# Performance work log

Hardware: AMD Instinct MI355X
Metric: run time of the kernel (lower is better)

The kernel has to match this reference:

```python
import jax, jax.numpy as jnp
import numpy as np

N_USERS, N_ITEMS, N_GROUPS = 20000, 20000, 2000
MAX_M, D, K, B = 20, 64, 2, 8192


def setup_inputs() -> dict:
    key = jax.random.key(0)
    ks = jax.random.split(key, 12)
    membership = jax.random.randint(ks[0], (N_GROUPS, MAX_M), 0, N_USERS)
    member_mask = jnp.zeros((N_GROUPS, MAX_M), jnp.float32)  # exp -> all-ones weights
    # binary group-member incidence consistent with membership (dedupes duplicates)
    hyper_graph = jnp.zeros((N_GROUPS, N_USERS), jnp.float32)
    hyper_graph = hyper_graph.at[jnp.arange(N_GROUPS)[:, None], membership].set(1.0)
    user_emb = 0.1 * jax.random.normal(ks[1], (N_USERS, D), jnp.float32)
    item_emb = 0.1 * jax.random.normal(ks[2], (N_ITEMS, D), jnp.float32)
    Wk = 0.05 * jax.random.normal(ks[3], (K, D, 2 * D), jnp.float32)
    bk = jnp.zeros((K, D), jnp.float32)
    p1w = 0.1 * jax.random.normal(ks[4], (16, D), jnp.float32)
    p1b = jnp.zeros((16,), jnp.float32)
    p2w = 0.1 * jax.random.normal(ks[5], (1, 16), jnp.float32)
    p2b = jnp.zeros((1,), jnp.float32)
    groups = jax.random.randint(ks[6], (B,), 0, N_GROUPS)
    items = jax.random.randint(ks[7], (B,), 0, N_ITEMS)
    return dict(groups=groups, items=items, membership=membership,
                member_mask=member_mask, hyper_graph=hyper_graph,
                user_emb=user_emb, item_emb=item_emb, Wk=Wk, bk=bk,
                p1w=p1w, p1b=p1b, p2w=p2w, p2b=p2b)


def _l2norm(x, eps=1e-12):
    return x / jnp.maximum(jnp.linalg.norm(x, axis=-1, keepdims=True), eps)


def reference(groups, items, membership, member_mask, hyper_graph,
              user_emb, item_emb, Wk, bk, p1w, p1b, p2w, p2b):
    # masked-mean group embedding from member users: [G, D]
    w = jnp.exp(member_mask)                                  # [G, M]
    g_users = user_emb[membership]                            # [G, M, D]
    emb = (g_users * w[..., None]).sum(1) / w.sum(1, keepdims=True)
    # group adjacency = common-member counts, zero diagonal
    adj = hyper_graph @ hyper_graph.T                         # [G, G]
    adj = adj - jnp.diag(jnp.diag(adj))
    # Vectorized set-intersection message: for binary H, common count == adj[i,j],
    # so sum_j adj[i,j] * mean(U[common(i,j)]) = sum_j (H_i * H_j) @ U (j != i)
    #                                          = (H * H.sum(0) - H) @ U
    deg = hyper_graph.sum(0)                                  # [n_users]
    neigh_member = (hyper_graph * deg[None, :] - hyper_graph) @ user_emb  # [G, D]
    for i in range(K):
        neigh_group = adj @ emb                               # [G, D]
        msg = neigh_group + neigh_member
        emb = jnp.concatenate([emb, msg], axis=1) @ Wk[i].T + bk[i]
        emb = _l2norm(emb)
    ge = emb[groups]                                          # [B, D]
    ie = item_emb[items]                                      # [B, D]
    h = jax.nn.relu((ge * ie) @ p1w.T + p1b)                  # [B, 16]
    return jax.nn.sigmoid(h @ p2w.T + p2b)                    # [B, 1]
```

## Files before the change

### kernel.cpp

```cpp
#include <hip/hip_runtime.h>
#include <math.h>

#define D 64
#define MAXM 20
#define CAP 32
#define CAPS 64
#define WPB 8
#define TPB 512

#define XOR_COMBINE4(v)                                        \
  do {                                                         \
    v.x += __shfl_xor(v.x, 16); v.x += __shfl_xor(v.x, 32);    \
    v.y += __shfl_xor(v.y, 16); v.y += __shfl_xor(v.y, 32);    \
    v.z += __shfl_xor(v.z, 16); v.z += __shfl_xor(v.z, 32);    \
    v.w += __shfl_xor(v.w, 16); v.w += __shfl_xor(v.w, 32);    \
  } while (0)

__global__ __launch_bounds__(TPB) void init_kernel(
    const int* __restrict__ membership, const float* __restrict__ member_mask,
    const float* __restrict__ user_emb, const int* __restrict__ groups,
    float* __restrict__ emb0, unsigned int* __restrict__ ufm,
    int* __restrict__ deg, int* __restrict__ inv,
    int* __restrict__ scnt, int* __restrict__ sidx, int G, int B) {
  const int w    = threadIdx.x >> 6;
  const int lane = threadIdx.x & 63;
  const int g    = blockIdx.x * WPB + w;
  const int sub  = lane >> 4, q = lane & 15;
  __shared__ int   mem_s[WPB][MAXM];
  __shared__ float wgt_s[WPB][MAXM];
  int*   mem = mem_s[w];
  float* wgt = wgt_s[w];
  if (g < G) {
    if (lane < MAXM) {
      mem[lane] = membership[g * MAXM + lane];
      wgt[lane] = expf(member_mask[g * MAXM + lane]);
    }
    float wsum = 0.f;
#pragma unroll
    for (int m = 0; m < MAXM; ++m) wsum += wgt[m];
    float4 acc = make_float4(0.f, 0.f, 0.f, 0.f);
#pragma unroll
    for (int it = 0; it < MAXM / 4; ++it) {
      const int m = it * 4 + sub;
      const float c = wgt[m];
      const float4 v = *(const float4*)(user_emb + (long)mem[m] * D + q * 4);
      acc.x += c * v.x; acc.y += c * v.y; acc.z += c * v.z; acc.w += c * v.w;
    }
    XOR_COMBINE4(acc);
    if (lane < 16) {
      const float iw = 1.f / wsum;
      float4 r = make_float4(acc.x * iw, acc.y * iw, acc.z * iw, acc.w * iw);
      ((float4*)(emb0 + (long)g * D))[q] = r;
    }
    bool uniq = false;
    if (lane < MAXM) {
      const int u = mem[lane];
      uniq = true;
      for (int m = 0; m < lane; ++m)
        if (mem[m] == u) uniq = false;
    }
    const unsigned long long bal = __ballot(uniq);
    if (lane == 0) ufm[g] = (unsigned int)bal;
    if (uniq) {
      const int u = mem[lane];
      const int pos = atomicAdd(&deg[u], 1);
      if (pos < CAP) inv[(long)u * CAP + pos] = g;
    }
  }
  const int nthreads = gridDim.x * TPB;
  for (int s = blockIdx.x * TPB + threadIdx.x; s < B; s += nthreads) {
    const int gg = groups[s];
    const int pos = atomicAdd(&scnt[gg], 1);
    if (pos < CAPS) sidx[gg * CAPS + pos] = s;
  }
}

__device__ __forceinline__ float update_core(
    const int* __restrict__ membership, const unsigned int* __restrict__ ufm,
    const int* __restrict__ deg, const int* __restrict__ inv,
    const float* __restrict__ user_emb, float* __restrict__ nm, int compute_nm,
    const float* __restrict__ Wk, const float* __restrict__ bk, int k,
    const float* __restrict__ cur, int g, int lane,
    int* mem, float* coef, float* e_sh, float* ms_sh, int* nbr) {
  const int sub = lane >> 4, q = lane & 15;
  if (lane < MAXM) mem[lane] = membership[g * MAXM + lane];
  const unsigned int um = ufm[g];
  const float ein = cur[(long)g * D + lane];
  e_sh[lane] = ein;

  int d = 0, u = 0;
  const bool uq = (lane < MAXM) && ((um >> lane) & 1u);
  if (uq) { u = mem[lane]; d = deg[u]; }
  if (lane < MAXM) coef[lane] = uq ? (float)(d - 1) : 0.f;
  const int dc = d < CAP ? d : CAP;
  int incl = dc;
#pragma unroll
  for (int off = 1; off < 64; off <<= 1) {
    const int v = __shfl_up(incl, off);
    if (lane >= off) incl += v;
  }
  const int total = __shfl(incl, 63);
  const int base = incl - dc;
  for (int i = 0; i < dc; ++i) nbr[base + i] = inv[(long)u * CAP + i];
  const int padc = (8 - (total & 7)) & 7;
  if (lane < padc) nbr[total + lane] = g;

  const int T8 = total + padc;
  float4 a0 = make_float4(0.f, 0.f, 0.f, 0.f);
  float4 a1 = make_float4(0.f, 0.f, 0.f, 0.f);
  for (int i = 0; i < T8; i += 8) {
    const int r0 = nbr[i + sub];
    const int r1 = nbr[i + 4 + sub];
    const float4 v0 = *(const float4*)(cur + (long)r0 * D + q * 4);
    const float4 v1 = *(const float4*)(cur + (long)r1 * D + q * 4);
    a0.x += v0.x; a0.y += v0.y; a0.z += v0.z; a0.w += v0.w;
    a1.x += v1.x; a1.y += v1.y; a1.z += v1.z; a1.w += v1.w;
  }
  float4 ng4 = make_float4(a0.x + a1.x, a0.y + a1.y, a0.z + a1.z, a0.w + a1.w);
  XOR_COMBINE4(ng4);

  float4 nm4 = make_float4(0.f, 0.f, 0.f, 0.f);
  if (compute_nm) {
#pragma unroll
    for (int it = 0; it < MAXM / 4; ++it) {
      const int m = it * 4 + sub;
      const float c = coef[m];
      const float4 v = *(const float4*)(user_emb + (long)mem[m] * D + q * 4);
      nm4.x += c * v.x; nm4.y += c * v.y; nm4.z += c * v.z; nm4.w += c * v.w;
    }
    XOR_COMBINE4(nm4);
    if (lane < 16) ((float4*)(nm + (long)g * D))[q] = nm4;
  }
  if (lane < 16) {
    const float4 nmv4 =
        compute_nm ? nm4 : ((const float4*)(nm + (long)g * D))[q];
    const float alpha = (float)__popc(um) + (float)padc;
    const float4 e4 = ((const float4*)e_sh)[q];
    float4 ms4;
    ms4.x = ng4.x + nmv4.x - alpha * e4.x;
    ms4.y = ng4.y + nmv4.y - alpha * e4.y;
    ms4.z = ng4.z + nmv4.z - alpha * e4.z;
    ms4.w = ng4.w + nmv4.w - alpha * e4.w;
    ((float4*)ms_sh)[q] = ms4;
  }

  const float4* W4 = (const float4*)(Wk + ((long)k * D + lane) * (2 * D));
  const float4* e4p = (const float4*)e_sh;
  const float4* m4p = (const float4*)ms_sh;
  float o = bk[k * D + lane];
#pragma unroll
  for (int j = 0; j < 16; ++j) {
    const float4 a = e4p[j], wv = W4[j];
    o += a.x * wv.x + a.y * wv.y + a.z * wv.z + a.w * wv.w;
  }
#pragma unroll
  for (int j = 0; j < 16; ++j) {
    const float4 a = m4p[j], wv = W4[16 + j];
    o += a.x * wv.x + a.y * wv.y + a.z * wv.z + a.w * wv.w;
  }
  float ss = o * o;
#pragma unroll
  for (int sh = 32; sh; sh >>= 1) ss += __shfl_xor(ss, sh);
  return o * (1.f / fmaxf(sqrtf(ss), 1e-12f));
}

__global__ __launch_bounds__(TPB) void upd_kernel(
    const int* __restrict__ membership, const unsigned int* __restrict__ ufm,
    const int* __restrict__ deg, const int* __restrict__ inv,
    const float* __restrict__ user_emb, float* __restrict__ nm, int compute_nm,
    const float* __restrict__ Wk, const float* __restrict__ bk, int k,
    const float* __restrict__ cur, float* __restrict__ nxt, int G) {
  const int w = threadIdx.x >> 6, lane = threadIdx.x & 63;
  const int g0 = blockIdx.x * WPB + w;
  const int g = g0 < G ? g0 : G - 1;
  __shared__ int   mem_s[WPB][MAXM];
  __shared__ float coef_s[WPB][MAXM];
  __shared__ float e_s[WPB][D], ms_s[WPB][D];
  __shared__ int   nbr_s[WPB][MAXM * CAP + 8];
  const float o = update_core(membership, ufm, deg, inv, user_emb, nm,
                              compute_nm, Wk, bk, k, cur, g, lane,
                              mem_s[w], coef_s[w], e_s[w], ms_s[w], nbr_s[w]);
  if (g0 < G) nxt[(long)g0 * D + lane] = o;
}

__global__ __launch_bounds__(TPB) void upd_head_kernel(
    const int* __restrict__ membership, const unsigned int* __restrict__ ufm,
    const int* __restrict__ deg, const int* __restrict__ inv,
    const float* __restrict__ user_emb, float* __restrict__ nm, int compute_nm,
    const float* __restrict__ Wk, const float* __restrict__ bk, int k,
    const float* __restrict__ cur,
    const int* __restrict__ scnt, const int* __restrict__ sidx,
    const int* __restrict__ items, const float* __restrict__ item_emb,
    const float* __restrict__ p1w, const float* __restrict__ p1b,
    const float* __restrict__ p2w, const float* __restrict__ p2b,
    float* __restrict__ out, int G) {
  const int w = threadIdx.x >> 6, lane = threadIdx.x & 63;
  const int g0 = blockIdx.x * WPB + w;
  const int g = g0 < G ? g0 : G - 1;
  __shared__ int   mem_s[WPB][MAXM];
  __shared__ float coef_s[WPB][MAXM];
  __shared__ float e_s[WPB][D], ms_s[WPB][D];
  __shared__ int   nbr_s[WPB][MAXM * CAP + 8];
  const float o = update_core(membership, ufm, deg, inv, user_emb, nm,
                              compute_nm, Wk, bk, k, cur, g, lane,
                              mem_s[w], coef_s[w], e_s[w], ms_s[w], nbr_s[w]);

  __shared__ float o_sh[WPB][D];
  __shared__ int   slist[WPB * CAPS];
  __shared__ unsigned char sgw[WPB * CAPS];
  __shared__ int   soff[WPB + 1];
  __shared__ int   scnt_sh[WPB];
  o_sh[w][lane] = o;
  if (lane == 0) scnt_sh[w] = (g0 < G) ? min(scnt[g0], CAPS) : 0;
  __syncthreads();
  if (threadIdx.x == 0) {
    soff[0] = 0;
    for (int i = 0; i < WPB; ++i) soff[i + 1] = soff[i] + scnt_sh[i];
  }
  __syncthreads();
  const int my = scnt_sh[w];
  for (int i = lane; i < my; i += 64) {
    slist[soff[w] + i] = sidx[g0 * CAPS + i];
    sgw[soff[w] + i] = (unsigned char)w;
  }
  __syncthreads();
  const int T = soff[WPB];
  if (T == 0) return;
  float p1r[16], p1br[16], p2wr[16];
#pragma unroll
  for (int j = 0; j < 16; ++j) {
    p1r[j]  = p1w[j * D + lane];
    p1br[j] = p1b[j];
    p2wr[j] = p2w[j];
  }
  const float p2b0 = p2b[0];
  for (int e = w; e < T; e += WPB) {
    const int s = slist[e];
    const int gw2 = sgw[e];
    const float x = o_sh[gw2][lane] * item_emb[(long)items[s] * D + lane];
    float pv[16];
#pragma unroll
    for (int j = 0; j < 16; ++j) pv[j] = x * p1r[j];
#pragma unroll
    for (int off = 32; off; off >>= 1) {
#pragma unroll
      for (int j = 0; j < 16; ++j) pv[j] += __shfl_xor(pv[j], off);
    }
    float acc2 = p2b0;
#pragma unroll
    for (int j = 0; j < 16; ++j)
      acc2 += fmaxf(pv[j] + p1br[j], 0.f) * p2wr[j];
    if (lane == 0) out[s] = 1.f / (1.f + expf(-acc2));
  }
}

extern "C" void kernel_launch(void* const* d_in, const int* in_sizes, int n_in,
                              void* d_out, int out_size, void* d_ws, size_t ws_size,
                              hipStream_t stream) {
  const int*   groups      = (const int*)d_in[0];
  const int*   items       = (const int*)d_in[1];
  const int*   membership  = (const int*)d_in[2];
  const float* member_mask = (const float*)d_in[3];
  const float* user_emb    = (const float*)d_in[5];
  const float* item_emb    = (const float*)d_in[6];
  const float* Wk          = (const float*)d_in[7];
  const float* bk          = (const float*)d_in[8];
  const float* p1w         = (const float*)d_in[9];
  const float* p1b         = (const float*)d_in[10];
  const float* p2w         = (const float*)d_in[11];
  const float* p2b         = (const float*)d_in[12];
  float* out = (float*)d_out;

  const int B  = in_sizes[0];
  const int G  = in_sizes[2] / MAXM;
  const int NU = in_sizes[5] / D;
  const int K  = in_sizes[7] / (D * 2 * D);

  char* ws = (char*)d_ws;
  float*        emb_a = (float*)ws;        ws += (size_t)G * D * 4;
  float*        emb_b = (float*)ws;        ws += (size_t)G * D * 4;
  float*        nm    = (float*)ws;        ws += (size_t)G * D * 4;
  int*          deg   = (int*)ws;          ws += (size_t)NU * 4;
  int*          scnt  = (int*)ws;          ws += (size_t)G * 4;
  int*          inv   = (int*)ws;          ws += (size_t)NU * CAP * 4;
  int*          sidx  = (int*)ws;          ws += (size_t)G * CAPS * 4;
  unsigned int* ufm   = (unsigned int*)ws; ws += (size_t)G * 4;

  const int nblk = (G + WPB - 1) / WPB;

  hipMemsetAsync(deg, 0, (size_t)(NU + G) * 4, stream);
  init_kernel<<<nblk, TPB, 0, stream>>>(membership, member_mask, user_emb,
                                        groups, emb_a, ufm, deg, inv,
                                        scnt, sidx, G, B);

  float* cur = emb_a;
  float* nxt = emb_b;
  for (int k = 0; k < K - 1; ++k) {
    upd_kernel<<<nblk, TPB, 0, stream>>>(membership, ufm, deg, inv, user_emb,
                                         nm, (k == 0) ? 1 : 0, Wk, bk, k,
                                         cur, nxt, G);
    float* tmp = cur; cur = nxt; nxt = tmp;
  }
  upd_head_kernel<<<nblk, TPB, 0, stream>>>(
      membership, ufm, deg, inv, user_emb, nm, (K == 1) ? 1 : 0, Wk, bk, K - 1,
      cur, scnt, sidx, items, item_emb, p1w, p1b, p2w, p2b, out, G);
}
```

Before: 57.13 us.

## Fuse init, update and head kernels into one cooperative kernel with grid barriers

Replaces the three-kernel sequence (init, per-layer update, head) with a single cooperative kernel that uses atomic-counter grid barriers between phases. Per-group state (unique-member mask, neighbour list, neigh_member vector, alpha) stays in registers and shared memory across layers, so ufm and nm are no longer written to or read back from global memory. This removes kernel launch gaps and some global traffic. In exchange it needs all 250 blocks of 512 threads resident at once and pays for spin-wait barriers.

```diff
diff --git a/kernel.cpp b/kernel.cpp
--- a/kernel.cpp
+++ b/kernel.cpp
@@ -16,194 +16,178 @@
     v.w += __shfl_xor(v.w, 16); v.w += __shfl_xor(v.w, 32);    \
   } while (0)
 
-__global__ __launch_bounds__(TPB) void init_kernel(
+__device__ __forceinline__ void grid_barrier(int* bar, int idx, int nblk) {
+  __syncthreads();
+  if (threadIdx.x == 0) {
+    int* cnt  = bar + idx * 32;
+    int* flag = bar + idx * 32 + 16;
+    __threadfence();
+    const int prev = __hip_atomic_fetch_add(cnt, 1, __ATOMIC_ACQ_REL,
+                                            __HIP_MEMORY_SCOPE_AGENT);
+    if (prev == nblk - 1) {
+      __hip_atomic_store(flag, 1, __ATOMIC_RELEASE, __HIP_MEMORY_SCOPE_AGENT);
+    } else {
+      while (__hip_atomic_load(flag, __ATOMIC_RELAXED,
+                               __HIP_MEMORY_SCOPE_AGENT) == 0)
+        __builtin_amdgcn_s_sleep(2);
+    }
+    __threadfence();
+  }
+  __syncthreads();
+}
+
+__global__ __launch_bounds__(TPB) void fused_kernel(
+    const int* __restrict__ groups, const int* __restrict__ items,
     const int* __restrict__ membership, const float* __restrict__ member_mask,
-    const float* __restrict__ user_emb, const int* __restrict__ groups,
-    float* __restrict__ emb0, unsigned int* __restrict__ ufm,
-    int* __restrict__ deg, int* __restrict__ inv,
-    int* __restrict__ scnt, int* __restrict__ sidx, int G, int B) {
-  const int w    = threadIdx.x >> 6;
-  const int lane = threadIdx.x & 63;
-  const int g    = blockIdx.x * WPB + w;
-  const int sub  = lane >> 4, q = lane & 15;
+    const float* __restrict__ user_emb, const float* __restrict__ item_emb,
+    const float* __restrict__ Wk, const float* __restrict__ bk,
+    const float* __restrict__ p1w, const float* __restrict__ p1b,
+    const float* __restrict__ p2w, const float* __restrict__ p2b,
+    float* __restrict__ out, float* __restrict__ emb_a,
+    float* __restrict__ emb_b, int* __restrict__ bar, int* __restrict__ deg,
+    int* __restrict__ inv, int* __restrict__ scnt, int* __restrict__ sidx,
+    int G, int NU, int B, int K) {
+  const int w = threadIdx.x >> 6, lane = threadIdx.x & 63;
+  const int g0 = blockIdx.x * WPB + w;
+  const int g = (g0 < G) ? g0 : G - 1;
+  const int sub = lane >> 4, q = lane & 15;
+  const int nblk = gridDim.x;
+
   __shared__ int   mem_s[WPB][MAXM];
-  __shared__ float wgt_s[WPB][MAXM];
-  int*   mem = mem_s[w];
-  float* wgt = wgt_s[w];
-  if (g < G) {
-    if (lane < MAXM) {
-      mem[lane] = membership[g * MAXM + lane];
-      wgt[lane] = expf(member_mask[g * MAXM + lane]);
-    }
-    float wsum = 0.f;
-#pragma unroll
-    for (int m = 0; m < MAXM; ++m) wsum += wgt[m];
-    float4 acc = make_float4(0.f, 0.f, 0.f, 0.f);
-#pragma unroll
-    for (int it = 0; it < MAXM / 4; ++it) {
-      const int m = it * 4 + sub;
-      const float c = wgt[m];
-      const float4 v = *(const float4*)(user_emb + (long)mem[m] * D + q * 4);
-      acc.x += c * v.x; acc.y += c * v.y; acc.z += c * v.z; acc.w += c * v.w;
-    }
-    XOR_COMBINE4(acc);
-    if (lane < 16) {
-      const float iw = 1.f / wsum;
-      float4 r = make_float4(acc.x * iw, acc.y * iw, acc.z * iw, acc.w * iw);
-      ((float4*)(emb0 + (long)g * D))[q] = r;
-    }
-    bool uniq = false;
-    if (lane < MAXM) {
-      const int u = mem[lane];
-      uniq = true;
-      for (int m = 0; m < lane; ++m)
-        if (mem[m] == u) uniq = false;
-    }
-    const unsigned long long bal = __ballot(uniq);
-    if (lane == 0) ufm[g] = (unsigned int)bal;
-    if (uniq) {
-      const int u = mem[lane];
-      const int pos = atomicAdd(&deg[u], 1);
-      if (pos < CAP) inv[(long)u * CAP + pos] = g;
-    }
-  }
-  const int nthreads = gridDim.x * TPB;
+  __shared__ float coef_s[WPB][MAXM];
+  __shared__ float e_s[WPB][D], ms_s[WPB][D];
+  __shared__ int   nbr_s[WPB][MAXM * CAP + 8];
+  int*   mem   = mem_s[w];
+  float* coef  = coef_s[w];
+  float* e_sh  = e_s[w];
+  float* ms_sh = ms_s[w];
+  int*   nbr   = nbr_s[w];
+
+  if (lane < MAXM) {
+    mem[lane]  = membership[g * MAXM + lane];
+    coef[lane] = expf(member_mask[g * MAXM + lane]);
+  }
+  float wsum = 0.f;
+#pragma unroll
+  for (int m = 0; m < MAXM; ++m) wsum += coef[m];
+  float4 acc = make_float4(0.f, 0.f, 0.f, 0.f);
+#pragma unroll
+  for (int it = 0; it < MAXM / 4; ++it) {
+    const int m = it * 4 + sub;
+    const float c = coef[m];
+    const float4 v = *(const float4*)(user_emb + (long)mem[m] * D + q * 4);
+    acc.x += c * v.x; acc.y += c * v.y; acc.z += c * v.z; acc.w += c * v.w;
+  }
+  XOR_COMBINE4(acc);
+  if (g0 < G && lane < 16) {
+    const float iw = 1.f / wsum;
+    ((float4*)(emb_a + (long)g0 * D))[q] =
+        make_float4(acc.x * iw, acc.y * iw, acc.z * iw, acc.w * iw);
+  }
+  bool uniq = false;
+  if (g0 < G && lane < MAXM) {
+    const int u = mem[lane];
+    uniq = true;
+    for (int m = 0; m < lane; ++m)
+      if (mem[m] == u) uniq = false;
+  }
+  const unsigned int um = (unsigned int)__ballot(uniq);
+  if (uniq) {
+    const int u = mem[lane];
+    const int pos = atomicAdd(&deg[u], 1);
+    if (pos < CAP) inv[(long)u * CAP + pos] = g0;
+  }
+  const int nthreads = nblk * TPB;
   for (int s = blockIdx.x * TPB + threadIdx.x; s < B; s += nthreads) {
     const int gg = groups[s];
     const int pos = atomicAdd(&scnt[gg], 1);
     if (pos < CAPS) sidx[gg * CAPS + pos] = s;
   }
-}
-
-__device__ __forceinline__ float update_core(
-    const int* __restrict__ membership, const unsigned int* __restrict__ ufm,
-    const int* __restrict__ deg, const int* __restrict__ inv,
-    const float* __restrict__ user_emb, float* __restrict__ nm, int compute_nm,
-    const float* __restrict__ Wk, const float* __restrict__ bk, int k,
-    const float* __restrict__ cur, int g, int lane,
-    int* mem, float* coef, float* e_sh, float* ms_sh, int* nbr) {
-  const int sub = lane >> 4, q = lane & 15;
-  if (lane < MAXM) mem[lane] = membership[g * MAXM + lane];
-  const unsigned int um = ufm[g];
-  const float ein = cur[(long)g * D + lane];
-  e_sh[lane] = ein;
-
-  int d = 0, u = 0;
-  const bool uq = (lane < MAXM) && ((um >> lane) & 1u);
-  if (uq) { u = mem[lane]; d = deg[u]; }
-  if (lane < MAXM) coef[lane] = uq ? (float)(d - 1) : 0.f;
-  const int dc = d < CAP ? d : CAP;
-  int incl = dc;
-#pragma unroll
-  for (int off = 1; off < 64; off <<= 1) {
-    const int v = __shfl_up(incl, off);
-    if (lane >= off) incl += v;
-  }
-  const int total = __shfl(incl, 63);
-  const int base = incl - dc;
-  for (int i = 0; i < dc; ++i) nbr[base + i] = inv[(long)u * CAP + i];
-  const int padc = (8 - (total & 7)) & 7;
-  if (lane < padc) nbr[total + lane] = g;
-
-  const int T8 = total + padc;
-  float4 a0 = make_float4(0.f, 0.f, 0.f, 0.f);
-  float4 a1 = make_float4(0.f, 0.f, 0.f, 0.f);
-  for (int i = 0; i < T8; i += 8) {
-    const int r0 = nbr[i + sub];
-    const int r1 = nbr[i + 4 + sub];
-    const float4 v0 = *(const float4*)(cur + (long)r0 * D + q * 4);
-    const float4 v1 = *(const float4*)(cur + (long)r1 * D + q * 4);
-    a0.x += v0.x; a0.y += v0.y; a0.z += v0.z; a0.w += v0.w;
-    a1.x += v1.x; a1.y += v1.y; a1.z += v1.z; a1.w += v1.w;
-  }
-  float4 ng4 = make_float4(a0.x + a1.x, a0.y + a1.y, a0.z + a1.z, a0.w + a1.w);
-  XOR_COMBINE4(ng4);
-
-  float4 nm4 = make_float4(0.f, 0.f, 0.f, 0.f);
-  if (compute_nm) {
-#pragma unroll
-    for (int it = 0; it < MAXM / 4; ++it) {
-      const int m = it * 4 + sub;
-      const float c = coef[m];
-      const float4 v = *(const float4*)(user_emb + (long)mem[m] * D + q * 4);
-      nm4.x += c * v.x; nm4.y += c * v.y; nm4.z += c * v.z; nm4.w += c * v.w;
-    }
-    XOR_COMBINE4(nm4);
-    if (lane < 16) ((float4*)(nm + (long)g * D))[q] = nm4;
-  }
-  if (lane < 16) {
-    const float4 nmv4 =
-        compute_nm ? nm4 : ((const float4*)(nm + (long)g * D))[q];
-    const float alpha = (float)__popc(um) + (float)padc;
-    const float4 e4 = ((const float4*)e_sh)[q];
-    float4 ms4;
-    ms4.x = ng4.x + nmv4.x - alpha * e4.x;
-    ms4.y = ng4.y + nmv4.y - alpha * e4.y;
-    ms4.z = ng4.z + nmv4.z - alpha * e4.z;
-    ms4.w = ng4.w + nmv4.w - alpha * e4.w;
-    ((float4*)ms_sh)[q] = ms4;
-  }
-
-  const float4* W4 = (const float4*)(Wk + ((long)k * D + lane) * (2 * D));
-  const float4* e4p = (const float4*)e_sh;
-  const float4* m4p = (const float4*)ms_sh;
-  float o = bk[k * D + lane];
-#pragma unroll
-  for (int j = 0; j < 16; ++j) {
-    const float4 a = e4p[j], wv = W4[j];
-    o += a.x * wv.x + a.y * wv.y + a.z * wv.z + a.w * wv.w;
-  }
-#pragma unroll
-  for (int j = 0; j < 16; ++j) {
-    const float4 a = m4p[j], wv = W4[16 + j];
-    o += a.x * wv.x + a.y * wv.y + a.z * wv.z + a.w * wv.w;
-  }
-  float ss = o * o;
-#pragma unroll
-  for (int sh = 32; sh; sh >>= 1) ss += __shfl_xor(ss, sh);
-  return o * (1.f / fmaxf(sqrtf(ss), 1e-12f));
-}
-
-__global__ __launch_bounds__(TPB) void upd_kernel(
-    const int* __restrict__ membership, const unsigned int* __restrict__ ufm,
-    const int* __restrict__ deg, const int* __restrict__ inv,
-    const float* __restrict__ user_emb, float* __restrict__ nm, int compute_nm,
-    const float* __restrict__ Wk, const float* __restrict__ bk, int k,
-    const float* __restrict__ cur, float* __restrict__ nxt, int G) {
-  const int w = threadIdx.x >> 6, lane = threadIdx.x & 63;
-  const int g0 = blockIdx.x * WPB + w;
-  const int g = g0 < G ? g0 : G - 1;
-  __shared__ int   mem_s[WPB][MAXM];
-  __shared__ float coef_s[WPB][MAXM];
-  __shared__ float e_s[WPB][D], ms_s[WPB][D];
-  __shared__ int   nbr_s[WPB][MAXM * CAP + 8];
-  const float o = update_core(membership, ufm, deg, inv, user_emb, nm,
-                              compute_nm, Wk, bk, k, cur, g, lane,
-                              mem_s[w], coef_s[w], e_s[w], ms_s[w], nbr_s[w]);
-  if (g0 < G) nxt[(long)g0 * D + lane] = o;
-}
-
-__global__ __launch_bounds__(TPB) void upd_head_kernel(
-    const int* __restrict__ membership, const unsigned int* __restrict__ ufm,
-    const int* __restrict__ deg, const int* __restrict__ inv,
-    const float* __restrict__ user_emb, float* __restrict__ nm, int compute_nm,
-    const float* __restrict__ Wk, const float* __restrict__ bk, int k,
-    const float* __restrict__ cur,
-    const int* __restrict__ scnt, const int* __restrict__ sidx,
-    const int* __restrict__ items, const float* __restrict__ item_emb,
-    const float* __restrict__ p1w, const float* __restrict__ p1b,
-    const float* __restrict__ p2w, const float* __restrict__ p2b,
-    float* __restrict__ out, int G) {
-  const int w = threadIdx.x >> 6, lane = threadIdx.x & 63;
-  const int g0 = blockIdx.x * WPB + w;
-  const int g = g0 < G ? g0 : G - 1;
-  __shared__ int   mem_s[WPB][MAXM];
-  __shared__ float coef_s[WPB][MAXM];
-  __shared__ float e_s[WPB][D], ms_s[WPB][D];
-  __shared__ int   nbr_s[WPB][MAXM * CAP + 8];
-  const float o = update_core(membership, ufm, deg, inv, user_emb, nm,
-                              compute_nm, Wk, bk, k, cur, g, lane,
-                              mem_s[w], coef_s[w], e_s[w], ms_s[w], nbr_s[w]);
+
+  float* cur = emb_a;
+  float* nxt = emb_b;
+  int total = 0, padc = 0;
+  float alpha = 0.f;
+  float4 nmreg = make_float4(0.f, 0.f, 0.f, 0.f);
+  float o = 0.f;
+  for (int k = 0; k < K; ++k) {
+    grid_barrier(bar, k, nblk);
+    const float ein = cur[(long)g * D + lane];
+    e_sh[lane] = ein;
+    if (k == 0) {
+      int d = 0, u = 0;
+      const bool uq = (lane < MAXM) && ((um >> lane) & 1u);
+      if (uq) { u = mem[lane]; d = deg[u]; }
+      if (lane < MAXM) coef[lane] = uq ? (float)(d - 1) : 0.f;
+      const int dc = d < CAP ? d : CAP;
+      int incl = dc;
+#pragma unroll
+      for (int off = 1; off < 64; off <<= 1) {
+        const int v = __shfl_up(incl, off);
+        if (lane >= off) incl += v;
+      }
+      total = __shfl(incl, 63);
+      const int base = incl - dc;
+      for (int i = 0; i < dc; ++i) nbr[base + i] = inv[(long)u * CAP + i];
+      padc = (8 - (total & 7)) & 7;
+      if (lane < padc) nbr[total + lane] = g;
+      alpha = (float)__popc(um) + (float)padc;
+#pragma unroll
+      for (int it = 0; it < MAXM / 4; ++it) {
+        const int m = it * 4 + sub;
+        const float c = coef[m];
+        const float4 v = *(const float4*)(user_emb + (long)mem[m] * D + q * 4);
+        nmreg.x += c * v.x; nmreg.y += c * v.y;
+        nmreg.z += c * v.z; nmreg.w += c * v.w;
+      }
+      XOR_COMBINE4(nmreg);
+    }
+    const int T8 = total + padc;
+    float4 a0 = make_float4(0.f, 0.f, 0.f, 0.f);
+    float4 a1 = make_float4(0.f, 0.f, 0.f, 0.f);
+    for (int i = 0; i < T8; i += 8) {
+      const int r0 = nbr[i + sub];
+      const int r1 = nbr[i + 4 + sub];
+      const float4 v0 = *(const float4*)(cur + (long)r0 * D + q * 4);
+      const float4 v1 = *(const float4*)(cur + (long)r1 * D + q * 4);
+      a0.x += v0.x; a0.y += v0.y; a0.z += v0.z; a0.w += v0.w;
+      a1.x += v1.x; a1.y += v1.y; a1.z += v1.z; a1.w += v1.w;
+    }
+    float4 ng4 =
+        make_float4(a0.x + a1.x, a0.y + a1.y, a0.z + a1.z, a0.w + a1.w);
+    XOR_COMBINE4(ng4);
+    if (lane < 16) {
+      const float4 e4 = ((const float4*)e_sh)[q];
+      float4 ms4;
+      ms4.x = ng4.x + nmreg.x - alpha * e4.x;
+      ms4.y = ng4.y + nmreg.y - alpha * e4.y;
+      ms4.z = ng4.z + nmreg.z - alpha * e4.z;
+      ms4.w = ng4.w + nmreg.w - alpha * e4.w;
+      ((float4*)ms_sh)[q] = ms4;
+    }
+    const float4* W4 = (const float4*)(Wk + ((long)k * D + lane) * (2 * D));
+    const float4* e4p = (const float4*)e_sh;
+    const float4* m4p = (const float4*)ms_sh;
+    float oo = bk[k * D + lane];
+#pragma unroll
+    for (int j = 0; j < 16; ++j) {
+      const float4 a = e4p[j], wv = W4[j];
+      oo += a.x * wv.x + a.y * wv.y + a.z * wv.z + a.w * wv.w;
+    }
+#pragma unroll
+    for (int j = 0; j < 16; ++j) {
+      const float4 a = m4p[j], wv = W4[16 + j];
+      oo += a.x * wv.x + a.y * wv.y + a.z * wv.z + a.w * wv.w;
+    }
+    float ss = oo * oo;
+#pragma unroll
+    for (int sh = 32; sh; sh >>= 1) ss += __shfl_xor(ss, sh);
+    o = oo * (1.f / fmaxf(sqrtf(ss), 1e-12f));
+    if (k + 1 < K) {
+      if (g0 < G) nxt[(long)g0 * D + lane] = o;
+      float* t = cur; cur = nxt; nxt = t;
+    }
+  }
 
   __shared__ float o_sh[WPB][D];
   __shared__ int   slist[WPB * CAPS];
@@ -211,7 +195,10 @@
   __shared__ int   soff[WPB + 1];
   __shared__ int   scnt_sh[WPB];
   o_sh[w][lane] = o;
-  if (lane == 0) scnt_sh[w] = (g0 < G) ? min(scnt[g0], CAPS) : 0;
+  if (lane == 0) {
+    int c = (g0 < G) ? scnt[g0] : 0;
+    scnt_sh[w] = c < CAPS ? c : CAPS;
+  }
   __syncthreads();
   if (threadIdx.x == 0) {
     soff[0] = 0;
@@ -271,37 +258,32 @@
   const float* p2b         = (const float*)d_in[12];
   float* out = (float*)d_out;
 
-  const int B  = in_sizes[0];
-  const int G  = in_sizes[2] / MAXM;
-  const int NU = in_sizes[5] / D;
-  const int K  = in_sizes[7] / (D * 2 * D);
+  int B  = in_sizes[0];
+  int G  = in_sizes[2] / MAXM;
+  int NU = in_sizes[5] / D;
+  int K  = in_sizes[7] / (D * 2 * D);
 
   char* ws = (char*)d_ws;
-  float*        emb_a = (float*)ws;        ws += (size_t)G * D * 4;
-  float*        emb_b = (float*)ws;        ws += (size_t)G * D * 4;
-  float*        nm    = (float*)ws;        ws += (size_t)G * D * 4;
+  int*          bar   = (int*)ws;          ws += 256 * 4;
   int*          deg   = (int*)ws;          ws += (size_t)NU * 4;
   int*          scnt  = (int*)ws;          ws += (size_t)G * 4;
   int*          inv   = (int*)ws;          ws += (size_t)NU * CAP * 4;
   int*          sidx  = (int*)ws;          ws += (size_t)G * CAPS * 4;
-  unsigned int* ufm   = (unsigned int*)ws; ws += (size_t)G * 4;
+  float*        emb_a = (float*)ws;        ws += (size_t)G * D * 4;
+  float*        emb_b = (float*)ws;        ws += (size_t)G * D * 4;
 
   const int nblk = (G + WPB - 1) / WPB;
 
-  hipMemsetAsync(deg, 0, (size_t)(NU + G) * 4, stream);
-  init_kernel<<<nblk, TPB, 0, stream>>>(membership, member_mask, user_emb,
-                                        groups, emb_a, ufm, deg, inv,
-                                        scnt, sidx, G, B);
-
-  float* cur = emb_a;
-  float* nxt = emb_b;
-  for (int k = 0; k < K - 1; ++k) {
-    upd_kernel<<<nblk, TPB, 0, stream>>>(membership, ufm, deg, inv, user_emb,
-                                         nm, (k == 0) ? 1 : 0, Wk, bk, k,
-                                         cur, nxt, G);
-    float* tmp = cur; cur = nxt; nxt = tmp;
-  }
-  upd_head_kernel<<<nblk, TPB, 0, stream>>>(
-      membership, ufm, deg, inv, user_emb, nm, (K == 1) ? 1 : 0, Wk, bk, K - 1,
-      cur, scnt, sidx, items, item_emb, p1w, p1b, p2w, p2b, out, G);
+  hipMemsetAsync(bar, 0, (size_t)(256 + NU + G) * 4, stream);
+
+  void* args[] = {
+    (void*)&groups, (void*)&items, (void*)&membership, (void*)&member_mask,
+    (void*)&user_emb, (void*)&item_emb, (void*)&Wk, (void*)&bk,
+    (void*)&p1w, (void*)&p1b, (void*)&p2w, (void*)&p2b,
+    (void*)&out, (void*)&emb_a, (void*)&emb_b, (void*)&bar,
+    (void*)&deg, (void*)&inv, (void*)&scnt, (void*)&sidx,
+    (void*)&G, (void*)&NU, (void*)&B, (void*)&K
+  };
+  hipLaunchCooperativeKernel((const void*)fused_kernel, dim3(nblk), dim3(TPB),
+                             args, 0, stream);
 }
```

After: 104.0 us. 1.82x slower.

## Build per-group neighbor lists in init via shared-memory hash scan, drop global atomics

Applied to the files above, without the earlier changes.

Replaces the global inverted index (per-user degree atomics and inverse lists, plus the memset) with a per-block approach. Each block hashes its groups' members into a shared-memory table, then scans the entire membership array to build each group's neighbor list, materialized into a flat per-group array. The neighbor-member term and the batch-sample lists are also computed in init, so the update kernels only read the precomputed lists and nm. The cost is that every one of ~250 blocks scans all 40k membership entries and the 8192 groups entries, which shifts substantial redundant work into init.

```diff
diff --git a/kernel.cpp b/kernel.cpp
--- a/kernel.cpp
+++ b/kernel.cpp
@@ -7,6 +7,8 @@
 #define CAPS 64
 #define WPB 8
 #define TPB 512
+#define HSZ 512
+#define NBRW (MAXM * CAP + 8)
 
 #define XOR_COMBINE4(v)                                        \
   do {                                                         \
@@ -19,22 +21,37 @@
 __global__ __launch_bounds__(TPB) void init_kernel(
     const int* __restrict__ membership, const float* __restrict__ member_mask,
     const float* __restrict__ user_emb, const int* __restrict__ groups,
-    float* __restrict__ emb0, unsigned int* __restrict__ ufm,
-    int* __restrict__ deg, int* __restrict__ inv,
-    int* __restrict__ scnt, int* __restrict__ sidx, int G, int B) {
+    float* __restrict__ emb0, float* __restrict__ nm, int* __restrict__ hdr,
+    int* __restrict__ nbrflat, int* __restrict__ scnt, int* __restrict__ sidx,
+    int G, int B) {
   const int w    = threadIdx.x >> 6;
   const int lane = threadIdx.x & 63;
-  const int g    = blockIdx.x * WPB + w;
+  const int g0   = blockIdx.x * WPB + w;
+  const int g    = (g0 < G) ? g0 : G - 1;
   const int sub  = lane >> 4, q = lane & 15;
+
   __shared__ int   mem_s[WPB][MAXM];
   __shared__ float wgt_s[WPB][MAXM];
+  __shared__ int   hkey[HSZ];
+  __shared__ int   hval[HSZ];
+  __shared__ int   lcnt[WPB * MAXM];
+  __shared__ int   lists[WPB * MAXM][CAP];
+  __shared__ int   scl[WPB];
+  __shared__ int   slist[WPB][CAPS];
   int*   mem = mem_s[w];
   float* wgt = wgt_s[w];
-  if (g < G) {
-    if (lane < MAXM) {
-      mem[lane] = membership[g * MAXM + lane];
-      wgt[lane] = expf(member_mask[g * MAXM + lane]);
-    }
+
+  if (g0 < G && lane < MAXM) {
+    mem[lane] = membership[g0 * MAXM + lane];
+    wgt[lane] = expf(member_mask[g0 * MAXM + lane]);
+  }
+  for (int i = threadIdx.x; i < HSZ; i += TPB) hkey[i] = -1;
+  for (int i = threadIdx.x; i < WPB * MAXM; i += TPB) lcnt[i] = 0;
+  if (threadIdx.x < WPB) scl[threadIdx.x] = 0;
+  __syncthreads();
+
+  unsigned int um = 0u;
+  if (g0 < G) {
     float wsum = 0.f;
 #pragma unroll
     for (int m = 0; m < MAXM; ++m) wsum += wgt[m];
@@ -49,8 +66,8 @@
     XOR_COMBINE4(acc);
     if (lane < 16) {
       const float iw = 1.f / wsum;
-      float4 r = make_float4(acc.x * iw, acc.y * iw, acc.z * iw, acc.w * iw);
-      ((float4*)(emb0 + (long)g * D))[q] = r;
+      ((float4*)(emb0 + (long)g0 * D))[q] =
+          make_float4(acc.x * iw, acc.y * iw, acc.z * iw, acc.w * iw);
     }
     bool uniq = false;
     if (lane < MAXM) {
@@ -59,49 +76,104 @@
       for (int m = 0; m < lane; ++m)
         if (mem[m] == u) uniq = false;
     }
-    const unsigned long long bal = __ballot(uniq);
-    if (lane == 0) ufm[g] = (unsigned int)bal;
+    um = (unsigned int)__ballot(uniq);
     if (uniq) {
       const int u = mem[lane];
-      const int pos = atomicAdd(&deg[u], 1);
-      if (pos < CAP) inv[(long)u * CAP + pos] = g;
-    }
-  }
-  const int nthreads = gridDim.x * TPB;
-  for (int s = blockIdx.x * TPB + threadIdx.x; s < B; s += nthreads) {
-    const int gg = groups[s];
-    const int pos = atomicAdd(&scnt[gg], 1);
-    if (pos < CAPS) sidx[gg * CAPS + pos] = s;
-  }
-}
-
-__device__ __forceinline__ float update_core(
-    const int* __restrict__ membership, const unsigned int* __restrict__ ufm,
-    const int* __restrict__ deg, const int* __restrict__ inv,
-    const float* __restrict__ user_emb, float* __restrict__ nm, int compute_nm,
-    const float* __restrict__ Wk, const float* __restrict__ bk, int k,
-    const float* __restrict__ cur, int g, int lane,
-    int* mem, float* coef, float* e_sh, float* ms_sh, int* nbr) {
+      unsigned h = ((unsigned)u * 2654435761u) & (HSZ - 1);
+      for (;;) {
+        const int old = atomicCAS(&hkey[h], -1, u);
+        if (old == -1) { hval[h] = w * MAXM + lane; break; }
+        h = (h + 1) & (HSZ - 1);
+      }
+    }
+  }
+  __syncthreads();
+
+  const int TOT = G * MAXM;
+  for (int e = threadIdx.x; e < TOT; e += TPB) {
+    const int u = membership[e];
+    unsigned h = ((unsigned)u * 2654435761u) & (HSZ - 1);
+    int key = hkey[h];
+    if (key == -1) continue;
+    int first = -1;
+    do {
+      if (key == u) {
+        if (first < 0) {
+          first = 1;
+          const int r0 = (e / MAXM) * MAXM;
+          for (int mm = r0; mm < e; ++mm)
+            if (membership[mm] == u) { first = 0; break; }
+        }
+        if (first) {
+          const int eidx = hval[h];
+          const int pos = atomicAdd(&lcnt[eidx], 1);
+          if (pos < CAP) lists[eidx][pos] = e / MAXM;
+        }
+      }
+      h = (h + 1) & (HSZ - 1);
+      key = hkey[h];
+    } while (key != -1);
+  }
+  const int base_g = blockIdx.x * WPB;
+  for (int s = threadIdx.x; s < B; s += TPB) {
+    const unsigned rel = (unsigned)(groups[s] - base_g);
+    if (rel < WPB) {
+      const int pos = atomicAdd(&scl[rel], 1);
+      if (pos < CAPS) slist[rel][pos] = s;
+    }
+  }
+  __syncthreads();
+
+  if (g0 < G) {
+    int deg_t = 0, dc = 0;
+    const bool uq = (lane < MAXM) && ((um >> lane) & 1u);
+    if (uq) {
+      deg_t = lcnt[w * MAXM + lane];
+      dc = deg_t < CAP ? deg_t : CAP;
+    }
+    const float coef = uq ? (float)(deg_t - 1) : 0.f;
+    wgt[lane < MAXM ? lane : 0] = (lane < MAXM) ? coef : wgt[0];
+    int incl = dc;
+#pragma unroll
+    for (int off = 1; off < 64; off <<= 1) {
+      const int v = __shfl_up(incl, off);
+      if (lane >= off) incl += v;
+    }
+    const int total = __shfl(incl, 63);
+    const int base = incl - dc;
+    for (int i = 0; i < dc; ++i)
+      nbrflat[(long)g0 * NBRW + base + i] = lists[w * MAXM + lane][i];
+    float4 nm4 = make_float4(0.f, 0.f, 0.f, 0.f);
+#pragma unroll
+    for (int it = 0; it < MAXM / 4; ++it) {
+      const int m = it * 4 + sub;
+      const float c = wgt[m];
+      const float4 v = *(const float4*)(user_emb + (long)mem[m] * D + q * 4);
+      nm4.x += c * v.x; nm4.y += c * v.y; nm4.z += c * v.z; nm4.w += c * v.w;
+    }
+    XOR_COMBINE4(nm4);
+    if (lane < 16) ((float4*)(nm + (long)g0 * D))[q] = nm4;
+    if (lane == 0) {
+      hdr[2 * g0]     = total;
+      hdr[2 * g0 + 1] = __popc(um);
+      scnt[g0] = scl[w] < CAPS ? scl[w] : CAPS;
+    }
+    const int ns = scl[w] < CAPS ? scl[w] : CAPS;
+    for (int i = lane; i < ns; i += 64) sidx[g0 * CAPS + i] = slist[w][i];
+  }
+}
+
+__device__ __forceinline__ float upd_core(
+    const int* __restrict__ hdr, const int* __restrict__ nbrflat,
+    const float* __restrict__ nm, const float* __restrict__ Wk,
+    const float* __restrict__ bk, int k, const float* __restrict__ cur,
+    int g, int lane, float* e_sh, float* ms_sh, int* nbr) {
   const int sub = lane >> 4, q = lane & 15;
-  if (lane < MAXM) mem[lane] = membership[g * MAXM + lane];
-  const unsigned int um = ufm[g];
+  const int total = hdr[2 * g];
+  const int ucnt  = hdr[2 * g + 1];
   const float ein = cur[(long)g * D + lane];
   e_sh[lane] = ein;
-
-  int d = 0, u = 0;
-  const bool uq = (lane < MAXM) && ((um >> lane) & 1u);
-  if (uq) { u = mem[lane]; d = deg[u]; }
-  if (lane < MAXM) coef[lane] = uq ? (float)(d - 1) : 0.f;
-  const int dc = d < CAP ? d : CAP;
-  int incl = dc;
-#pragma unroll
-  for (int off = 1; off < 64; off <<= 1) {
-    const int v = __shfl_up(incl, off);
-    if (lane >= off) incl += v;
-  }
-  const int total = __shfl(incl, 63);
-  const int base = incl - dc;
-  for (int i = 0; i < dc; ++i) nbr[base + i] = inv[(long)u * CAP + i];
+  for (int i = lane; i < total; i += 64) nbr[i] = nbrflat[(long)g * NBRW + i];
   const int padc = (8 - (total & 7)) & 7;
   if (lane < padc) nbr[total + lane] = g;
 
@@ -119,22 +191,9 @@
   float4 ng4 = make_float4(a0.x + a1.x, a0.y + a1.y, a0.z + a1.z, a0.w + a1.w);
   XOR_COMBINE4(ng4);
 
-  float4 nm4 = make_float4(0.f, 0.f, 0.f, 0.f);
-  if (compute_nm) {
-#pragma unroll
-    for (int it = 0; it < MAXM / 4; ++it) {
-      const int m = it * 4 + sub;
-      const float c = coef[m];
-      const float4 v = *(const float4*)(user_emb + (long)mem[m] * D + q * 4);
-      nm4.x += c * v.x; nm4.y += c * v.y; nm4.z += c * v.z; nm4.w += c * v.w;
-    }
-    XOR_COMBINE4(nm4);
-    if (lane < 16) ((float4*)(nm + (long)g * D))[q] = nm4;
-  }
   if (lane < 16) {
-    const float4 nmv4 =
-        compute_nm ? nm4 : ((const float4*)(nm + (long)g * D))[q];
-    const float alpha = (float)__popc(um) + (float)padc;
+    const float4 nmv4 = ((const float4*)(nm + (long)g * D))[q];
+    const float alpha = (float)ucnt + (float)padc;
     const float4 e4 = ((const float4*)e_sh)[q];
     float4 ms4;
     ms4.x = ng4.x + nmv4.x - alpha * e4.x;
@@ -165,30 +224,24 @@
 }
 
 __global__ __launch_bounds__(TPB) void upd_kernel(
-    const int* __restrict__ membership, const unsigned int* __restrict__ ufm,
-    const int* __restrict__ deg, const int* __restrict__ inv,
-    const float* __restrict__ user_emb, float* __restrict__ nm, int compute_nm,
-    const float* __restrict__ Wk, const float* __restrict__ bk, int k,
-    const float* __restrict__ cur, float* __restrict__ nxt, int G) {
+    const int* __restrict__ hdr, const int* __restrict__ nbrflat,
+    const float* __restrict__ nm, const float* __restrict__ Wk,
+    const float* __restrict__ bk, int k, const float* __restrict__ cur,
+    float* __restrict__ nxt, int G) {
   const int w = threadIdx.x >> 6, lane = threadIdx.x & 63;
   const int g0 = blockIdx.x * WPB + w;
   const int g = g0 < G ? g0 : G - 1;
-  __shared__ int   mem_s[WPB][MAXM];
-  __shared__ float coef_s[WPB][MAXM];
   __shared__ float e_s[WPB][D], ms_s[WPB][D];
-  __shared__ int   nbr_s[WPB][MAXM * CAP + 8];
-  const float o = update_core(membership, ufm, deg, inv, user_emb, nm,
-                              compute_nm, Wk, bk, k, cur, g, lane,
-                              mem_s[w], coef_s[w], e_s[w], ms_s[w], nbr_s[w]);
+  __shared__ int   nbr_s[WPB][NBRW];
+  const float o = upd_core(hdr, nbrflat, nm, Wk, bk, k, cur, g, lane,
+                           e_s[w], ms_s[w], nbr_s[w]);
   if (g0 < G) nxt[(long)g0 * D + lane] = o;
 }
 
 __global__ __launch_bounds__(TPB) void upd_head_kernel(
-    const int* __restrict__ membership, const unsigned int* __restrict__ ufm,
-    const int* __restrict__ deg, const int* __restrict__ inv,
-    const float* __restrict__ user_emb, float* __restrict__ nm, int compute_nm,
-    const float* __restrict__ Wk, const float* __restrict__ bk, int k,
-    const float* __restrict__ cur,
+    const int* __restrict__ hdr, const int* __restrict__ nbrflat,
+    const float* __restrict__ nm, const float* __restrict__ Wk,
+    const float* __restrict__ bk, int k, const float* __restrict__ cur,
     const int* __restrict__ scnt, const int* __restrict__ sidx,
     const int* __restrict__ items, const float* __restrict__ item_emb,
     const float* __restrict__ p1w, const float* __restrict__ p1b,
@@ -197,13 +250,10 @@
   const int w = threadIdx.x >> 6, lane = threadIdx.x & 63;
   const int g0 = blockIdx.x * WPB + w;
   const int g = g0 < G ? g0 : G - 1;
-  __shared__ int   mem_s[WPB][MAXM];
-  __shared__ float coef_s[WPB][MAXM];
   __shared__ float e_s[WPB][D], ms_s[WPB][D];
-  __shared__ int   nbr_s[WPB][MAXM * CAP + 8];
-  const float o = update_core(membership, ufm, deg, inv, user_emb, nm,
-                              compute_nm, Wk, bk, k, cur, g, lane,
-                              mem_s[w], coef_s[w], e_s[w], ms_s[w], nbr_s[w]);
+  __shared__ int   nbr_s[WPB][NBRW];
+  const float o = upd_core(hdr, nbrflat, nm, Wk, bk, k, cur, g, lane,
+                           e_s[w], ms_s[w], nbr_s[w]);
 
   __shared__ float o_sh[WPB][D];
   __shared__ int   slist[WPB * CAPS];
@@ -273,35 +323,31 @@
 
   const int B  = in_sizes[0];
   const int G  = in_sizes[2] / MAXM;
-  const int NU = in_sizes[5] / D;
   const int K  = in_sizes[7] / (D * 2 * D);
 
   char* ws = (char*)d_ws;
-  float*        emb_a = (float*)ws;        ws += (size_t)G * D * 4;
-  float*        emb_b = (float*)ws;        ws += (size_t)G * D * 4;
-  float*        nm    = (float*)ws;        ws += (size_t)G * D * 4;
-  int*          deg   = (int*)ws;          ws += (size_t)NU * 4;
-  int*          scnt  = (int*)ws;          ws += (size_t)G * 4;
-  int*          inv   = (int*)ws;          ws += (size_t)NU * CAP * 4;
-  int*          sidx  = (int*)ws;          ws += (size_t)G * CAPS * 4;
-  unsigned int* ufm   = (unsigned int*)ws; ws += (size_t)G * 4;
+  float* emb_a   = (float*)ws; ws += (size_t)G * D * 4;
+  float* emb_b   = (float*)ws; ws += (size_t)G * D * 4;
+  float* nm      = (float*)ws; ws += (size_t)G * D * 4;
+  int*   hdr     = (int*)ws;   ws += (size_t)G * 2 * 4;
+  int*   nbrflat = (int*)ws;   ws += (size_t)G * NBRW * 4;
+  int*   scnt    = (int*)ws;   ws += (size_t)G * 4;
+  int*   sidx    = (int*)ws;   ws += (size_t)G * CAPS * 4;
 
   const int nblk = (G + WPB - 1) / WPB;
 
-  hipMemsetAsync(deg, 0, (size_t)(NU + G) * 4, stream);
   init_kernel<<<nblk, TPB, 0, stream>>>(membership, member_mask, user_emb,
-                                        groups, emb_a, ufm, deg, inv,
+                                        groups, emb_a, nm, hdr, nbrflat,
                                         scnt, sidx, G, B);
 
   float* cur = emb_a;
   float* nxt = emb_b;
   for (int k = 0; k < K - 1; ++k) {
-    upd_kernel<<<nblk, TPB, 0, stream>>>(membership, ufm, deg, inv, user_emb,
-                                         nm, (k == 0) ? 1 : 0, Wk, bk, k,
+    upd_kernel<<<nblk, TPB, 0, stream>>>(hdr, nbrflat, nm, Wk, bk, k,
                                          cur, nxt, G);
     float* tmp = cur; cur = nxt; nxt = tmp;
   }
   upd_head_kernel<<<nblk, TPB, 0, stream>>>(
-      membership, ufm, deg, inv, user_emb, nm, (K == 1) ? 1 : 0, Wk, bk, K - 1,
-      cur, scnt, sidx, items, item_emb, p1w, p1b, p2w, p2b, out, G);
-}
+      hdr, nbrflat, nm, Wk, bk, K - 1, cur, scnt, sidx, items, item_emb,
+      p1w, p1b, p2w, p2b, out, G);
+}
```

Result: slower. 184.3 us (+222.7%).
